# Optimization experiments

Measured on AMD Instinct MI355X. Metric: run time of the kernel, lower is better.

The kernel has to match this reference:

```python
import jax, jax.numpy as jnp
import numpy as np

HIDDEN = 2048
HEADS = 16
HEAD_DIM = HIDDEN // HEADS
B, L = 4, 2048


def _rotate_half(x):
    x1, x2 = jnp.split(x, 2, axis=-1)
    return jnp.concatenate([-x2, x1], axis=-1)


def setup_inputs() -> dict:
    key = jax.random.key(0)
    k1, k2, k3 = jax.random.split(key, 3)
    x = jax.random.normal(k1, (B, L, HIDDEN), dtype=jnp.float32)
    # realistic rotary tables
    inv_freq = 1.0 / (10000.0 ** (jnp.arange(0, HEAD_DIM, 2, dtype=jnp.float32) / HEAD_DIM))
    t = jnp.arange(L, dtype=jnp.float32)
    freqs = jnp.outer(t, inv_freq)  # [L, HEAD_DIM/2]
    emb = jnp.concatenate([freqs, freqs], axis=-1)  # [L, HEAD_DIM]
    cos = jnp.cos(emb)
    sin = jnp.sin(emb)
    w_qkv = jax.random.normal(k2, (3 * HIDDEN, HIDDEN), dtype=jnp.float32) * (HIDDEN ** -0.5)
    w_out = jax.random.normal(k3, (HIDDEN, HIDDEN), dtype=jnp.float32) * (HIDDEN ** -0.5)
    return {"x": x, "cos": cos, "sin": sin, "w_qkv": w_qkv, "w_out": w_out}


def reference(x, cos, sin, w_qkv, w_out):
    b, l, d = x.shape
    qkv = jnp.einsum('bld,ed->ble', x, w_qkv)  # [B, L, 3D]
    q, k, v = jnp.split(qkv, 3, axis=-1)
    # [B, H, L, Dh]
    q = q.reshape(b, l, HEADS, HEAD_DIM).transpose(0, 2, 1, 3)
    k = k.reshape(b, l, HEADS, HEAD_DIM).transpose(0, 2, 1, 3)
    v = v.reshape(b, l, HEADS, HEAD_DIM).transpose(0, 2, 1, 3)
    cos_ = cos[None, None, :l, :]
    sin_ = sin[None, None, :l, :]
    q = q * cos_ + _rotate_half(q) * sin_
    k = k * cos_ + _rotate_half(k) * sin_
    scale = 1.0 / jnp.sqrt(jnp.asarray(HEAD_DIM, dtype=q.dtype))
    scores = jnp.einsum('bhqd,bhkd->bhqk', q, k) * scale
    attn = jax.nn.softmax(scores, axis=-1)
    out = jnp.einsum('bhqk,bhkd->bhqd', attn, v)  # [B, H, L, Dh]
    out = out.transpose(0, 2, 1, 3).reshape(b, l, d)
    return jnp.einsum('bld,ed->ble', out, w_out)
```

## Files before the change

### kernel.cpp

```cpp
#include <hip/hip_runtime.h>
#include <cstdint>
#include <cstddef>

typedef unsigned short u16;
typedef __attribute__((ext_vector_type(8))) short bf16x8;
typedef __attribute__((ext_vector_type(4))) float f32x4;

#define DEVFN static __device__ __forceinline__

DEVFN u16 f2bf(float f) {
  unsigned u = __float_as_uint(f);
  unsigned r = (u + 0x7FFFu + ((u >> 16) & 1u)) >> 16;
  return (u16)r;
}

DEVFN void gload16(const void* g, void* l) {
  __builtin_amdgcn_global_load_lds(
      (const __attribute__((address_space(1))) void*)g,
      (__attribute__((address_space(3))) void*)l, 16, 0, 0);
}

#define WAITVM(n) asm volatile("s_waitcnt vmcnt(" #n ")" ::: "memory")
#define BARRIER() do { asm volatile("" ::: "memory"); \
                       __builtin_amdgcn_s_barrier();   \
                       asm volatile("" ::: "memory"); } while (0)

__global__ void prep(const float* __restrict__ x, const float* __restrict__ wqkv,
                     const float* __restrict__ wout, const float* __restrict__ cosp,
                     const float* __restrict__ sinp, u16* __restrict__ xb,
                     u16* __restrict__ wqkvb, u16* __restrict__ woutb,
                     float2* __restrict__ cs) {
  constexpr int X4 = 4194304;
  constexpr int W4 = 3145728;
  constexpr int O4 = 1048576;
  int i = blockIdx.x * blockDim.x + threadIdx.x;
  if (i < X4) {
    float4 v = ((const float4*)x)[i];
    unsigned long long w = (unsigned long long)f2bf(v.x)
        | ((unsigned long long)f2bf(v.y) << 16)
        | ((unsigned long long)f2bf(v.z) << 32)
        | ((unsigned long long)f2bf(v.w) << 48);
    *(unsigned long long*)(xb + (size_t)i * 4) = w;
  } else if (i < X4 + W4) {
    int j = i - X4;
    int base = j * 4;
    int e = base >> 11, col = base & 2047;
    int e2;
    if (e < 4096) {
      int part = e >> 11, loc = e & 2047;
      int h = loc >> 7, d = loc & 127;
      int d2 = (d < 64) ? 2 * d : 2 * (d - 64) + 1;
      e2 = part * 2048 + h * 128 + d2;
    } else {
      e2 = e;
    }
    float4 v = *(const float4*)&wqkv[(size_t)base];
    unsigned long long w = (unsigned long long)f2bf(v.x)
        | ((unsigned long long)f2bf(v.y) << 16)
        | ((unsigned long long)f2bf(v.z) << 32)
        | ((unsigned long long)f2bf(v.w) << 48);
    *(unsigned long long*)(wqkvb + (size_t)e2 * 2048 + col) = w;
  } else if (i < X4 + W4 + O4) {
    int j = i - X4 - W4;
    float4 v = ((const float4*)wout)[j];
    unsigned long long w = (unsigned long long)f2bf(v.x)
        | ((unsigned long long)f2bf(v.y) << 16)
        | ((unsigned long long)f2bf(v.z) << 32)
        | ((unsigned long long)f2bf(v.w) << 48);
    *(unsigned long long*)(woutb + (size_t)j * 4) = w;
  } else {
    int k = i - X4 - W4 - O4;
    int ld4 = k * 4;
#pragma unroll
    for (int u = 0; u < 4; u++) {
      int ld = ld4 + u;
      int l = ld >> 6, d = ld & 63;
      cs[ld] = make_float2(cosp[(size_t)l * 128 + d], sinp[(size_t)l * 128 + d]);
    }
  }
}

enum { M_F32OUT = 0, M_ROPE = 1, M_VT = 2 };

DEVFN bf16x8 rdfrag(const u16* buf, int row, int chunk) {
  return *(const bf16x8*)&buf[row * 64 + (((chunk ^ (row & 7)) & 7) << 3)];
}

template <int MODE, int Q>
DEVFN void phase_mfma(const u16* Ac, const u16* Bc, int wm, int wn, int quad, int l16,
                      bf16x8 (&bfr)[4][2], f32x4 (&acc)[8][4]) {
  if (Q == 0) {
#pragma unroll
    for (int j = 0; j < 4; j++)
#pragma unroll
      for (int kk = 0; kk < 2; kk++)
        bfr[j][kk] = rdfrag(Bc, wn * 64 + j * 16 + l16, kk * 4 + quad);
  }
  bf16x8 af[2][2];
#pragma unroll
  for (int i2 = 0; i2 < 2; i2++)
#pragma unroll
    for (int kk = 0; kk < 2; kk++)
      af[i2][kk] = rdfrag(Ac, wm * 128 + (Q * 2 + i2) * 16 + l16, kk * 4 + quad);
  __builtin_amdgcn_s_setprio(1);
#pragma unroll
  for (int kk = 0; kk < 2; kk++)
#pragma unroll
    for (int i2 = 0; i2 < 2; i2++)
#pragma unroll
      for (int j = 0; j < 4; j++) {
        if (MODE == M_VT)
          acc[Q * 2 + i2][j] = __builtin_amdgcn_mfma_f32_16x16x32_bf16(
              bfr[j][kk], af[i2][kk], acc[Q * 2 + i2][j], 0, 0, 0);
        else
          acc[Q * 2 + i2][j] = __builtin_amdgcn_mfma_f32_16x16x32_bf16(
              af[i2][kk], bfr[j][kk], acc[Q * 2 + i2][j], 0, 0, 0);
      }
  __builtin_amdgcn_s_setprio(0);
}

template <int MODE>
DEVFN void gemm256_core(const u16* __restrict__ A, const u16* __restrict__ Bt,
                        void* __restrict__ Cv, const float2* __restrict__ cs,
                        int N, int m0, int n0, u16* As, u16* Bs) {
  int tid = threadIdx.x;
  int wv = tid >> 6, lane = tid & 63, quad = lane >> 4, l16 = lane & 15;
  int wm = wv >> 2, wn = wv & 3;

  const u16* pB[2][2];
  const u16* pA[4];
#pragma unroll
  for (int h = 0; h < 2; h++)
#pragma unroll
    for (int o = 0; o < 2; o++) {
      int r = h * 128 + o * 64 + wv * 8 + (lane >> 3);
      int ck = (lane & 7) ^ (r & 7);
      pB[h][o] = Bt + (size_t)(n0 + r) * 2048 + ck * 8;
    }
#pragma unroll
  for (int q = 0; q < 4; q++) {
    int rb = (wv < 4) ? (q * 32 + wv * 8) : (128 + q * 32 + (wv - 4) * 8);
    int r = rb + (lane >> 3);
    int ck = (lane & 7) ^ (r & 7);
    pA[q] = A + (size_t)(m0 + r) * 2048 + ck * 8;
  }

#define STAGE_B(h, buf, kk) do {                                    \
    int rb0_ = (h) * 128 + wv * 8;                                  \
    gload16(pB[h][0] + (kk), &(buf)[rb0_ * 64]);                    \
    gload16(pB[h][1] + (kk), &(buf)[(rb0_ + 64) * 64]); } while (0)
#define STAGE_A(q, buf, kk) do {                                    \
    int rb_ = ((wv < 4) ? ((q) * 32 + wv * 8)                       \
                        : (128 + (q) * 32 + (wv - 4) * 8));         \
    gload16(pA[q] + (kk), &(buf)[rb_ * 64]); } while (0)

  f32x4 acc[8][4] = {};
  bf16x8 bfr[4][2];

  STAGE_B(0, Bs, 0);
  STAGE_B(1, Bs, 0);
  STAGE_A(0, As, 0);
  STAGE_A(1, As, 0);
  STAGE_A(2, As, 0);
  STAGE_A(3, As, 0);

  for (int t = 0; t < 31; t++) {
    const u16* Ac = As + (t & 1) * 16384;
    const u16* Bc = Bs + (t & 1) * 16384;
    u16* An = As + ((t + 1) & 1) * 16384;
    u16* Bn = Bs + ((t + 1) & 1) * 16384;
    int kn = (t + 1) * 64;
    STAGE_B(0, Bn, kn);
    WAITVM(5); BARRIER();
    phase_mfma<MODE, 0>(Ac, Bc, wm, wn, quad, l16, bfr, acc);
    STAGE_B(1, Bn, kn);
    WAITVM(6); BARRIER();
    phase_mfma<MODE, 1>(Ac, Bc, wm, wn, quad, l16, bfr, acc);
    STAGE_A(0, An, kn);
    STAGE_A(1, An, kn);
    WAITVM(7); BARRIER();
    phase_mfma<MODE, 2>(Ac, Bc, wm, wn, quad, l16, bfr, acc);
    STAGE_A(2, An, kn);
    STAGE_A(3, An, kn);
    WAITVM(8); BARRIER();
    phase_mfma<MODE, 3>(Ac, Bc, wm, wn, quad, l16, bfr, acc);
  }
  {
    const u16* Ac = As + 16384;
    const u16* Bc = Bs + 16384;
    WAITVM(3); BARRIER();
    phase_mfma<MODE, 0>(Ac, Bc, wm, wn, quad, l16, bfr, acc);
    WAITVM(2); BARRIER();
    phase_mfma<MODE, 1>(Ac, Bc, wm, wn, quad, l16, bfr, acc);
    WAITVM(1); BARRIER();
    phase_mfma<MODE, 2>(Ac, Bc, wm, wn, quad, l16, bfr, acc);
    WAITVM(0); BARRIER();
    phase_mfma<MODE, 3>(Ac, Bc, wm, wn, quad, l16, bfr, acc);
  }
#undef STAGE_B
#undef STAGE_A

  if (MODE == M_F32OUT) {
    float* C = (float*)Cv;
#pragma unroll
    for (int i = 0; i < 8; i++)
#pragma unroll
      for (int r = 0; r < 4; r++) {
        size_t row = (size_t)(m0 + wm * 128 + i * 16 + quad * 4 + r);
#pragma unroll
        for (int j = 0; j < 4; j++)
          C[row * N + (n0 + wn * 64 + j * 16 + l16)] = acc[i][j][r];
      }
  } else if (MODE == M_ROPE) {
    constexpr float QSCALE = 1.4426950408889634f * 0.08838834764831845f;
    const float scale = (n0 >> 11) ? 1.0f : QSCALE;
    u16* C = (u16*)Cv;
#pragma unroll
    for (int i = 0; i < 8; i++)
#pragma unroll
      for (int r = 0; r < 4; r++) {
        int row = m0 + wm * 128 + i * 16 + quad * 4 + r;
        int l = row & 2047;
#pragma unroll
        for (int j = 0; j < 4; j++) {
          int col = n0 + wn * 64 + j * 16 + l16;
          int dm = (col & 127) >> 1;
          float2 csv = cs[l * 64 + dm];
          float v = acc[i][j][r];
          float pv = __shfl_xor(v, 1);
          float sg = (l16 & 1) ? csv.y : -csv.y;
          C[(size_t)row * 4096 + col] = f2bf((v * csv.x + pv * sg) * scale);
        }
      }
  } else {
    u16* vt = (u16*)Cv;
#pragma unroll
    for (int j = 0; j < 4; j++)
#pragma unroll
      for (int r = 0; r < 4; r++) {
        int vch = n0 + wn * 64 + j * 16 + quad * 4 + r;
        int h = vch >> 7, d = vch & 127;
#pragma unroll
        for (int i = 0; i < 8; i++) {
          int token = m0 + wm * 128 + i * 16 + l16;
          int b = token >> 11, lloc = token & 2047;
          vt[((size_t)(b * 16 + h)) * 262144 + (size_t)d * 2048 + lloc] =
              f2bf(acc[i][j][r]);
        }
      }
  }
}

__global__ __launch_bounds__(512, 2) void gemm_qkv(const u16* __restrict__ xb,
                                                   const u16* __restrict__ wqkvb,
                                                   u16* __restrict__ qkvo,
                                                   u16* __restrict__ vto,
                                                   const float2* __restrict__ cs) {
  __shared__ u16 As[32768];
  __shared__ u16 Bs[32768];
  int id = blockIdx.x;
  int xcd = id & 7, sub = id >> 3;
  int bx = sub % 24, by = xcd * 4 + sub / 24;
  if (bx < 16)
    gemm256_core<M_ROPE>(xb, wqkvb, qkvo, cs, 0, by * 256, bx * 256, As, Bs);
  else
    gemm256_core<M_VT>(xb, wqkvb + (size_t)4096 * 2048, vto, nullptr, 0,
                       by * 256, (bx - 16) * 256, As, Bs);
}

__global__ __launch_bounds__(512, 2) void gemm_out_k(const u16* __restrict__ A,
                                                     const u16* __restrict__ Bt,
                                                     float* __restrict__ C) {
  __shared__ u16 As[32768];
  __shared__ u16 Bs[32768];
  int id = blockIdx.x;
  int xcd = id & 7, sub = id >> 3;
  int bx = sub % 8, by = xcd * 4 + sub / 8;
  gemm256_core<M_F32OUT>(A, Bt, C, nullptr, 2048, by * 256, bx * 256, As, Bs);
}

DEVFN int swz(int row, int chunk)   { return row * 128 + ((chunk ^ (row & 15)) << 3); }
DEVFN int swz64(int row, int chunk) { return row * 64  + ((chunk ^ (row & 7)) << 3); }

__global__ __launch_bounds__(512) void attn_fused(const u16* __restrict__ qkv,
                                                  const u16* __restrict__ vt,
                                                  u16* __restrict__ out) {
  __shared__ u16 S[40960];
  u16* const Pb = S + 32768;
  int tid = threadIdx.x;
  int wv = tid >> 6, lane = tid & 63, quad = lane >> 4, l16 = lane & 15;
  int id = blockIdx.x;
  int xcd = id & 7, sub = id >> 3;
  int bh = ((sub >> 4) << 3) | xcd;
  int qt = sub & 15;
  int b = bh >> 4, h = bh & 15;
  const u16* qptr = qkv + (size_t)b * 2048 * 4096 + h * 128;
  const u16* kptr = qptr + 2048;
  const u16* vptr = vt + (size_t)bh * 262144;
  int q0 = qt * 128;

#pragma unroll
  for (int j = 0; j < 4; j++) {
    int rb = wv * 4 + j * 32;
    int r = rb + (lane >> 4);
    int ck = (lane & 15) ^ (r & 15);
    gload16(&qptr[(size_t)(q0 + r) * 4096 + ck * 8], &S[rb * 128]);
  }
  __syncthreads();
  bf16x8 qf[4];
#pragma unroll
  for (int ks = 0; ks < 4; ks++)
    qf[ks] = *(const bf16x8*)&S[swz(wv * 16 + l16, ks * 4 + quad)];
  __syncthreads();

  f32x4 o[8] = {};
  float l[4] = {0.f, 0.f, 0.f, 0.f};

#pragma unroll
  for (int j = 0; j < 2; j++) {
    int rbk = wv * 4 + j * 32;
    int rk = rbk + (lane >> 4);
    int ckk = (lane & 15) ^ (rk & 15);
    gload16(&kptr[(size_t)rk * 4096 + ckk * 8], &S[rbk * 128]);
    int rbv = wv * 8 + j * 64;
    int rv = rbv + (lane >> 3);
    int ckv = (lane & 7) ^ (rv & 7);
    gload16(&vptr[(size_t)rv * 2048 + ckv * 8], &S[16384 + rbv * 64]);
  }

  for (int kt = 0; kt < 32; kt++) {
    int cur = kt & 1;
    const u16* Kc = S + cur * 8192;
    const u16* Vc = S + 16384 + cur * 8192;
    __syncthreads();
    if (kt < 31) {
      int kk0 = (kt + 1) * 64;
      u16* kb = S + (cur ^ 1) * 8192;
      u16* vb = S + 16384 + (cur ^ 1) * 8192;
#pragma unroll
      for (int j = 0; j < 2; j++) {
        int rbk = wv * 4 + j * 32;
        int rk = rbk + (lane >> 4);
        int ckk = (lane & 15) ^ (rk & 15);
        gload16(&kptr[(size_t)(kk0 + rk) * 4096 + ckk * 8], &kb[rbk * 128]);
        int rbv = wv * 8 + j * 64;
        int rv = rbv + (lane >> 3);
        int ckv = (lane & 7) ^ (rv & 7);
        gload16(&vptr[(size_t)rv * 2048 + kk0 + ckv * 8], &vb[rbv * 64]);
      }
    }
    f32x4 s[4] = {};
#pragma unroll
    for (int ks = 0; ks < 4; ks++) {
#pragma unroll
      for (int nt = 0; nt < 4; nt++) {
        bf16x8 bfr = *(const bf16x8*)&Kc[swz(nt * 16 + l16, ks * 4 + quad)];
        s[nt] = __builtin_amdgcn_mfma_f32_16x16x32_bf16(qf[ks], bfr, s[nt], 0, 0, 0);
      }
    }
#pragma unroll
    for (int nt = 0; nt < 4; nt++)
#pragma unroll
      for (int r = 0; r < 4; r++) {
        float p = exp2f(s[nt][r]);
        l[r] += p;
        int row = wv * 16 + quad * 4 + r;
        int col = nt * 16 + l16;
        Pb[swz64(row, col >> 3) + (col & 7)] = f2bf(p);
      }
#pragma unroll
    for (int ks = 0; ks < 2; ks++) {
      bf16x8 pf = *(const bf16x8*)&Pb[swz64(wv * 16 + l16, ks * 4 + quad)];
#pragma unroll
      for (int nt = 0; nt < 8; nt++) {
        bf16x8 vf = *(const bf16x8*)&Vc[swz64(nt * 16 + l16, ks * 4 + quad)];
        o[nt] = __builtin_amdgcn_mfma_f32_16x16x32_bf16(pf, vf, o[nt], 0, 0, 0);
      }
    }
  }
#pragma unroll
  for (int r = 0; r < 4; r++)
#pragma unroll
    for (int off = 1; off < 16; off <<= 1) l[r] += __shfl_xor(l[r], off, 16);
  u16* obase = out + ((size_t)b * 2048 + q0) * 2048 + h * 128;
#pragma unroll
  for (int r = 0; r < 4; r++) {
    float inv = 1.0f / l[r];
    int row = wv * 16 + quad * 4 + r;
#pragma unroll
    for (int nt = 0; nt < 8; nt++)
      obase[(size_t)row * 2048 + nt * 16 + l16] = f2bf(o[nt][r] * inv);
  }
}

extern "C" void kernel_launch(void* const* d_in, const int* in_sizes, int n_in,
                              void* d_out, int out_size, void* d_ws, size_t ws_size,
                              hipStream_t stream) {
  const float* x    = (const float*)d_in[0];
  const float* cosp = (const float*)d_in[1];
  const float* sinp = (const float*)d_in[2];
  const float* wqkv = (const float*)d_in[3];
  const float* wout = (const float*)d_in[4];
  float* outp = (float*)d_out;

  u16* ws    = (u16*)d_ws;
  u16* xb    = ws;
  u16* wqkvb = xb + 16777216;
  u16* woutb = wqkvb + 12582912;
  u16* qkv   = woutb + 4194304;
  u16* vt    = qkv + 33554432;
  float2* cs = (float2*)(vt + 16777216);
  u16* attn  = xb;

  prep<<<32896, 256, 0, stream>>>(x, wqkv, wout, cosp, sinp, xb, wqkvb, woutb, cs);
  gemm_qkv<<<768, 512, 0, stream>>>(xb, wqkvb, qkv, vt, cs);
  attn_fused<<<1024, 512, 0, stream>>>(qkv, vt, attn);
  gemm_out_k<<<256, 512, 0, stream>>>(attn, woutb, outp);
}
```

Baseline: 664.4 us.

## Restructure attention to 4 waves with 32 query rows each and 32-key tiles

The attention kernel now runs with 256 threads (4 waves), and each wave processes two 16-row query fragments, so every K and V fragment read from LDS feeds two MFMAs. The key tile shrinks from 64 to 32, which halves the LDS footprint and allows three blocks per CU, at the cost of twice as many loop iterations and barriers. The P buffer moves to a padded row layout instead of the swizzled one. An explicit lgkmcnt wait plus a sched barrier is added between the P writes and the P reads within each wave.

```diff
diff --git a/kernel.cpp b/kernel.cpp
--- a/kernel.cpp
+++ b/kernel.cpp
@@ -24,6 +24,8 @@
 #define BARRIER() do { asm volatile("" ::: "memory"); \
                        __builtin_amdgcn_s_barrier();   \
                        asm volatile("" ::: "memory"); } while (0)
+#define FENCE_LDS() do { asm volatile("s_waitcnt lgkmcnt(0)" ::: "memory"); \
+                         __builtin_amdgcn_sched_barrier(0); } while (0)
 
 __global__ void prep(const float* __restrict__ x, const float* __restrict__ wqkv,
                      const float* __restrict__ wout, const float* __restrict__ cosp,
@@ -280,117 +282,128 @@
 }
 
 DEVFN int swz(int row, int chunk)   { return row * 128 + ((chunk ^ (row & 15)) << 3); }
-DEVFN int swz64(int row, int chunk) { return row * 64  + ((chunk ^ (row & 7)) << 3); }
-
-__global__ __launch_bounds__(512) void attn_fused(const u16* __restrict__ qkv,
-                                                  const u16* __restrict__ vt,
-                                                  u16* __restrict__ out) {
-  __shared__ u16 S[40960];
-  u16* const Pb = S + 32768;
+DEVFN int swz32(int row, int chunk) { return row * 32  + (((chunk ^ (row & 3)) & 3) << 3); }
+
+__global__ __launch_bounds__(256, 3) void attn_fused(const u16* __restrict__ qkv,
+                                                     const u16* __restrict__ vt,
+                                                     u16* __restrict__ out) {
+  __shared__ u16 S[21504];
+  u16* const Pb = S + 16384;
   int tid = threadIdx.x;
   int wv = tid >> 6, lane = tid & 63, quad = lane >> 4, l16 = lane & 15;
   int id = blockIdx.x;
   int xcd = id & 7, sub = id >> 3;
   int bh = ((sub >> 4) << 3) | xcd;
   int qt = sub & 15;
-  int b = bh >> 4, h = bh & 15;
-  const u16* qptr = qkv + (size_t)b * 2048 * 4096 + h * 128;
+  int b = bh >> 4, hh = bh & 15;
+  const u16* qptr = qkv + (size_t)b * 2048 * 4096 + hh * 128;
   const u16* kptr = qptr + 2048;
   const u16* vptr = vt + (size_t)bh * 262144;
   int q0 = qt * 128;
 
 #pragma unroll
-  for (int j = 0; j < 4; j++) {
-    int rb = wv * 4 + j * 32;
+  for (int j = 0; j < 8; j++) {
+    int rb = wv * 4 + j * 16;
     int r = rb + (lane >> 4);
     int ck = (lane & 15) ^ (r & 15);
     gload16(&qptr[(size_t)(q0 + r) * 4096 + ck * 8], &S[rb * 128]);
   }
   __syncthreads();
-  bf16x8 qf[4];
-#pragma unroll
-  for (int ks = 0; ks < 4; ks++)
-    qf[ks] = *(const bf16x8*)&S[swz(wv * 16 + l16, ks * 4 + quad)];
+  bf16x8 qf[2][4];
+#pragma unroll
+  for (int hf = 0; hf < 2; hf++)
+#pragma unroll
+    for (int ks = 0; ks < 4; ks++)
+      qf[hf][ks] = *(const bf16x8*)&S[swz(wv * 32 + hf * 16 + l16, ks * 4 + quad)];
   __syncthreads();
 
-  f32x4 o[8] = {};
-  float l[4] = {0.f, 0.f, 0.f, 0.f};
+  f32x4 o[2][8] = {};
+  float l[2][4] = {{0.f, 0.f, 0.f, 0.f}, {0.f, 0.f, 0.f, 0.f}};
 
 #pragma unroll
   for (int j = 0; j < 2; j++) {
-    int rbk = wv * 4 + j * 32;
+    int rbk = wv * 4 + j * 16;
     int rk = rbk + (lane >> 4);
     int ckk = (lane & 15) ^ (rk & 15);
     gload16(&kptr[(size_t)rk * 4096 + ckk * 8], &S[rbk * 128]);
-    int rbv = wv * 8 + j * 64;
-    int rv = rbv + (lane >> 3);
-    int ckv = (lane & 7) ^ (rv & 7);
-    gload16(&vptr[(size_t)rv * 2048 + ckv * 8], &S[16384 + rbv * 64]);
-  }
-
-  for (int kt = 0; kt < 32; kt++) {
+    int rbv = wv * 16 + j * 64;
+    int rv = rbv + (lane >> 2);
+    int ckv = (lane & 3) ^ (rv & 3);
+    gload16(&vptr[(size_t)rv * 2048 + ckv * 8], &S[8192 + rbv * 32]);
+  }
+
+  for (int kt = 0; kt < 64; kt++) {
     int cur = kt & 1;
-    const u16* Kc = S + cur * 8192;
-    const u16* Vc = S + 16384 + cur * 8192;
+    const u16* Kc = S + cur * 4096;
+    const u16* Vc = S + 8192 + cur * 4096;
     __syncthreads();
-    if (kt < 31) {
-      int kk0 = (kt + 1) * 64;
-      u16* kb = S + (cur ^ 1) * 8192;
-      u16* vb = S + 16384 + (cur ^ 1) * 8192;
+    if (kt < 63) {
+      int kk0 = (kt + 1) * 32;
+      u16* kb = S + (cur ^ 1) * 4096;
+      u16* vb = S + 8192 + (cur ^ 1) * 4096;
 #pragma unroll
       for (int j = 0; j < 2; j++) {
-        int rbk = wv * 4 + j * 32;
+        int rbk = wv * 4 + j * 16;
         int rk = rbk + (lane >> 4);
         int ckk = (lane & 15) ^ (rk & 15);
         gload16(&kptr[(size_t)(kk0 + rk) * 4096 + ckk * 8], &kb[rbk * 128]);
-        int rbv = wv * 8 + j * 64;
-        int rv = rbv + (lane >> 3);
-        int ckv = (lane & 7) ^ (rv & 7);
-        gload16(&vptr[(size_t)rv * 2048 + kk0 + ckv * 8], &vb[rbv * 64]);
-      }
-    }
-    f32x4 s[4] = {};
+        int rbv = wv * 16 + j * 64;
+        int rv = rbv + (lane >> 2);
+        int ckv = (lane & 3) ^ (rv & 3);
+        gload16(&vptr[(size_t)rv * 2048 + kk0 + ckv * 8], &vb[rbv * 32]);
+      }
+    }
+    f32x4 s[2][2] = {};
 #pragma unroll
     for (int ks = 0; ks < 4; ks++) {
 #pragma unroll
-      for (int nt = 0; nt < 4; nt++) {
+      for (int nt = 0; nt < 2; nt++) {
         bf16x8 bfr = *(const bf16x8*)&Kc[swz(nt * 16 + l16, ks * 4 + quad)];
-        s[nt] = __builtin_amdgcn_mfma_f32_16x16x32_bf16(qf[ks], bfr, s[nt], 0, 0, 0);
-      }
-    }
-#pragma unroll
-    for (int nt = 0; nt < 4; nt++)
-#pragma unroll
-      for (int r = 0; r < 4; r++) {
-        float p = exp2f(s[nt][r]);
-        l[r] += p;
-        int row = wv * 16 + quad * 4 + r;
-        int col = nt * 16 + l16;
-        Pb[swz64(row, col >> 3) + (col & 7)] = f2bf(p);
-      }
-#pragma unroll
-    for (int ks = 0; ks < 2; ks++) {
-      bf16x8 pf = *(const bf16x8*)&Pb[swz64(wv * 16 + l16, ks * 4 + quad)];
+        s[0][nt] = __builtin_amdgcn_mfma_f32_16x16x32_bf16(qf[0][ks], bfr, s[0][nt], 0, 0, 0);
+        s[1][nt] = __builtin_amdgcn_mfma_f32_16x16x32_bf16(qf[1][ks], bfr, s[1][nt], 0, 0, 0);
+      }
+    }
+#pragma unroll
+    for (int hf = 0; hf < 2; hf++)
+#pragma unroll
+      for (int nt = 0; nt < 2; nt++)
+#pragma unroll
+        for (int r = 0; r < 4; r++) {
+          float p = exp2f(s[hf][nt][r]);
+          l[hf][r] += p;
+          int row = wv * 32 + hf * 16 + quad * 4 + r;
+          int col = nt * 16 + l16;
+          Pb[row * 40 + col] = f2bf(p);
+        }
+    FENCE_LDS();
+    {
+      bf16x8 pf0 = *(const bf16x8*)&Pb[(wv * 32 + l16) * 40 + quad * 8];
+      bf16x8 pf1 = *(const bf16x8*)&Pb[(wv * 32 + 16 + l16) * 40 + quad * 8];
 #pragma unroll
       for (int nt = 0; nt < 8; nt++) {
-        bf16x8 vf = *(const bf16x8*)&Vc[swz64(nt * 16 + l16, ks * 4 + quad)];
-        o[nt] = __builtin_amdgcn_mfma_f32_16x16x32_bf16(pf, vf, o[nt], 0, 0, 0);
-      }
-    }
-  }
-#pragma unroll
-  for (int r = 0; r < 4; r++)
-#pragma unroll
-    for (int off = 1; off < 16; off <<= 1) l[r] += __shfl_xor(l[r], off, 16);
-  u16* obase = out + ((size_t)b * 2048 + q0) * 2048 + h * 128;
-#pragma unroll
-  for (int r = 0; r < 4; r++) {
-    float inv = 1.0f / l[r];
-    int row = wv * 16 + quad * 4 + r;
-#pragma unroll
-    for (int nt = 0; nt < 8; nt++)
-      obase[(size_t)row * 2048 + nt * 16 + l16] = f2bf(o[nt][r] * inv);
-  }
+        bf16x8 vf = *(const bf16x8*)&Vc[swz32(nt * 16 + l16, quad)];
+        o[0][nt] = __builtin_amdgcn_mfma_f32_16x16x32_bf16(pf0, vf, o[0][nt], 0, 0, 0);
+        o[1][nt] = __builtin_amdgcn_mfma_f32_16x16x32_bf16(pf1, vf, o[1][nt], 0, 0, 0);
+      }
+    }
+  }
+#pragma unroll
+  for (int hf = 0; hf < 2; hf++)
+#pragma unroll
+    for (int r = 0; r < 4; r++)
+#pragma unroll
+      for (int off = 1; off < 16; off <<= 1) l[hf][r] += __shfl_xor(l[hf][r], off, 16);
+  u16* obase = out + ((size_t)b * 2048 + q0) * 2048 + hh * 128;
+#pragma unroll
+  for (int hf = 0; hf < 2; hf++)
+#pragma unroll
+    for (int r = 0; r < 4; r++) {
+      float inv = 1.0f / l[hf][r];
+      int row = wv * 32 + hf * 16 + quad * 4 + r;
+#pragma unroll
+      for (int nt = 0; nt < 8; nt++)
+        obase[(size_t)row * 2048 + nt * 16 + l16] = f2bf(o[hf][nt][r] * inv);
+    }
 }
 
 extern "C" void kernel_launch(void* const* d_in, const int* in_sizes, int n_in,
@@ -414,6 +427,6 @@
 
   prep<<<32896, 256, 0, stream>>>(x, wqkv, wout, cosp, sinp, xb, wqkvb, woutb, cs);
   gemm_qkv<<<768, 512, 0, stream>>>(xb, wqkvb, qkv, vt, cs);
-  attn_fused<<<1024, 512, 0, stream>>>(qkv, vt, attn);
+  attn_fused<<<1024, 256, 0, stream>>>(qkv, vt, attn);
   gemm_out_k<<<256, 512, 0, stream>>>(attn, woutb, outp);
 }
```

Result: faster. 616.9 us (-7.1%).
